# Optimization experiments

Hardware: AMD Instinct MI355X
Metric: run time of the kernel (lower is better)

The kernel has to match this reference:

```python
import jax, jax.numpy as jnp
import numpy as np

V, E, H, K = 50000, 256, 512, 32
START, STOP = 30, 31
B, T = 32, 256
NEG = -10000.0


def _lstm_dir(x, W_ih, W_hh, b, h0, c0):
    # x: [T,B,E] -> outputs [T,B,H]; PyTorch gate order i,f,g,o
    xw = jnp.einsum('tbe,ge->tbg', x, W_ih) + b  # [T,B,4H]
    def step(carry, xw_t):
        h, c = carry
        z = xw_t + h @ W_hh.T
        i, f, g, o = jnp.split(z, 4, axis=-1)
        c = jax.nn.sigmoid(f) * c + jax.nn.sigmoid(i) * jnp.tanh(g)
        h = jax.nn.sigmoid(o) * jnp.tanh(c)
        return (h, c), h
    (_, _), hs = jax.lax.scan(step, (h0, c0), xw)
    return hs


def setup_inputs() -> dict:
    key = jax.random.key(0)
    ks = jax.random.split(key, 13)
    sc = 0.05
    sentence = jax.random.randint(ks[0], (B, T), 0, V)
    emb = jax.random.normal(ks[1], (V, E), jnp.float32) * 0.1
    W_ih_f = jax.random.normal(ks[2], (4 * H, E), jnp.float32) * sc
    W_hh_f = jax.random.normal(ks[3], (4 * H, H), jnp.float32) * sc
    b_f = jax.random.normal(ks[4], (4 * H,), jnp.float32) * sc
    W_ih_b = jax.random.normal(ks[5], (4 * H, E), jnp.float32) * sc
    W_hh_b = jax.random.normal(ks[6], (4 * H, H), jnp.float32) * sc
    b_b = jax.random.normal(ks[7], (4 * H,), jnp.float32) * sc
    W_out = jax.random.normal(ks[8], (K, 2 * H), jnp.float32) * sc
    b_out = jax.random.normal(ks[9], (K,), jnp.float32) * sc
    transitions = jax.random.normal(ks[10], (K, K), jnp.float32)
    transitions = transitions.at[START, :].set(NEG).at[:, STOP].set(NEG)
    h0 = jax.random.normal(ks[11], (2, B, H), jnp.float32)
    c0 = jax.random.normal(ks[12], (2, B, H), jnp.float32)
    return dict(sentence=sentence, emb=emb, W_ih_f=W_ih_f, W_hh_f=W_hh_f, b_f=b_f,
                W_ih_b=W_ih_b, W_hh_b=W_hh_b, b_b=b_b, W_out=W_out, b_out=b_out,
                transitions=transitions, h0=h0, c0=c0)


def reference(sentence, emb, W_ih_f, W_hh_f, b_f, W_ih_b, W_hh_b, b_b,
              W_out, b_out, transitions, h0, c0):
    batch, seqlen = sentence.shape
    ntag = transitions.shape[0]
    # embedding (dropout = identity at inference), time-major
    x = emb[sentence].transpose(1, 0, 2)  # [T,B,E]
    hf = _lstm_dir(x, W_ih_f, W_hh_f, b_f, h0[0], c0[0])
    hb = _lstm_dir(x[::-1], W_ih_b, W_hh_b, b_b, h0[1], c0[1])[::-1]
    rnn_out = jnp.concatenate([hf, hb], axis=-1).transpose(1, 0, 2)  # [B,T,2H]
    feats = rnn_out @ W_out.T + b_out  # [B,T,K]

    # Viterbi decode, vectorized over batch and tags
    v0 = jnp.full((batch, ntag), NEG, feats.dtype).at[:, START].set(0.0)
    def vstep(v, feat_t):
        # scores[b, next, prev] = v[b, prev] + transitions[next, prev]
        scores = v[:, None, :] + transitions[None, :, :]
        bp = jnp.argmax(scores, axis=-1)              # [B,K] best prev per next
        v_new = jnp.max(scores, axis=-1) + feat_t     # [B,K]
        return v_new, bp
    v, bps = jax.lax.scan(vstep, v0, feats.transpose(1, 0, 2))  # bps: [T,B,K]

    terminal = v + transitions[STOP]                  # [B,K]
    best_last = jnp.argmax(terminal, axis=-1)         # [B]
    path_score = jnp.take_along_axis(terminal, best_last[:, None], axis=1)[:, 0]

    def back(tag, bp_t):
        prev = jnp.take_along_axis(bp_t, tag[:, None], axis=1)[:, 0]
        return prev, tag
    _, path = jax.lax.scan(back, best_last, bps, reverse=True)  # [T,B], time order
    best_path = path.transpose(1, 0)                  # [B,T]
    return path_score, best_path
```

## Files before the change

kernel.cpp:

```cpp
#include <hip/hip_runtime.h>
#include <hip/hip_bf16.h>
#include <cstdint>


typedef __attribute__((ext_vector_type(8)))  short          s8v;
typedef __attribute__((ext_vector_type(8)))  __bf16         bf8v;
typedef __attribute__((ext_vector_type(16))) float          f32x16;
typedef __attribute__((ext_vector_type(4)))  float          f32x4v;
typedef __attribute__((ext_vector_type(4)))  unsigned int   u32x4;
typedef __attribute__((ext_vector_type(8)))  unsigned short u16x8;
typedef __attribute__((ext_vector_type(4)))  unsigned short u16x4;

template <typename V>
static __device__ inline auto mfma_try(V a, V b, f32x16 c, int)
    -> decltype(__builtin_amdgcn_mfma_f32_32x32x16_bf16(a, b, c, 0, 0, 0)) {
  return __builtin_amdgcn_mfma_f32_32x32x16_bf16(a, b, c, 0, 0, 0);
}
template <typename V>
static __device__ inline f32x16 mfma_try(V a, V b, f32x16 c, long) {
  return __builtin_amdgcn_mfma_f32_32x32x16_bf16(
      __builtin_bit_cast(bf8v, a), __builtin_bit_cast(bf8v, b), c, 0, 0, 0);
}
static __device__ inline f32x16 mfma32(u16x8 a, u16x8 b, f32x16 c) {
  return mfma_try(__builtin_bit_cast(s8v, a), __builtin_bit_cast(s8v, b), c, 0);
}

static __device__ inline unsigned short bf_trunc(float x) {
  return (unsigned short)(__builtin_bit_cast(unsigned int, x) >> 16);
}
static __device__ inline float bf_up(unsigned short h) {
  return __builtin_bit_cast(float, ((unsigned int)h) << 16);
}
static __device__ inline void split2(float x, unsigned short& hi, unsigned short& lo) {
  hi = bf_trunc(x);
  lo = bf_trunc(x - bf_up(hi));
}
static __device__ inline float sigmoidf_(float x) { return 1.0f / (1.0f + __expf(-x)); }
static __device__ inline float tanhf_(float x) {
  float ax = fabsf(x);
  float e  = __expf(-2.0f * ax);
  float t  = (1.0f - e) / (1.0f + e);
  return x < 0.0f ? -t : t;
}

static __device__ inline u32x4 ld16(const void* p) {
  u32x4 r;
  asm volatile("global_load_dwordx4 %0, %1, off" : "=v"(r) : "v"(p) : "memory");
  return r;
}
static __device__ inline u32x4 ld_cohere16(const void* p) {
  u32x4 r;
  asm volatile("global_load_dwordx4 %0, %1, off sc0 sc1" : "=v"(r) : "v"(p) : "memory");
  return r;
}
static __device__ inline void st_cohere16(void* p, u32x4 v) {
  asm volatile("global_store_dwordx4 %0, %1, off sc0 sc1" :: "v"(p), "v"(v) : "memory");
}
static __device__ inline void st_cohere4(void* p, int v) {
  asm volatile("global_store_dword %0, %1, off sc0 sc1" :: "v"(p), "v"(v) : "memory");
}
#define WAITVM(N)                                              \
  do {                                                         \
    asm volatile("s_waitcnt vmcnt(" #N ")" ::: "memory");      \
    __builtin_amdgcn_sched_barrier(0);                         \
  } while (0)

__global__ void k_embed(const int* __restrict__ sent, const float* __restrict__ emb,
                        unsigned short* __restrict__ xhi, unsigned short* __restrict__ xlo) {
  int row  = blockIdx.x * 4 + (threadIdx.x >> 6);
  int lane = threadIdx.x & 63;
  int t = row >> 5, b = row & 31;
  int tok = sent[b * 256 + t];
  const f32x4v v = *(const f32x4v*)(emb + (long)tok * 256 + lane * 4);
  u16x4 h4, l4;
#pragma unroll
  for (int i = 0; i < 4; ++i) {
    unsigned short h, l;
    split2(v[i], h, l);
    h4[i] = h; l4[i] = l;
  }
  *(u16x4*)(xhi + (long)row * 256 + lane * 4) = h4;
  *(u16x4*)(xlo + (long)row * 256 + lane * 4) = l4;
}

__global__ __launch_bounds__(256, 1) void k_lstm(
    const float* __restrict__ Whh_f, const float* __restrict__ Whh_b,
    const float* __restrict__ Wih_f, const float* __restrict__ Wih_b,
    const float* __restrict__ b_f,   const float* __restrict__ b_b,
    const float* __restrict__ h0,    const float* __restrict__ c0,
    const unsigned short* __restrict__ xhi, const unsigned short* __restrict__ xlo,
    unsigned short* __restrict__ hist, int* __restrict__ flags) {
  const int tid = threadIdx.x, lane = tid & 63, w = tid >> 6;
  const int blk = blockIdx.x, dir = blk >> 6, b64 = blk & 63;
  const float* Whh  = dir ? Whh_b : Whh_f;
  const float* Wih  = dir ? Wih_b : Wih_f;
  const float* bias = dir ? b_b   : b_f;

  __shared__ float zp[4][32][33];
  __shared__ __align__(16) unsigned short hstage[512];

  const int n  = lane & 31;
  const int kh = lane >> 5;
  const int wrow = ((n >> 3) << 9) + (b64 << 3) + (n & 7);

  u16x8 wbh[8], wbl[8];
#pragma unroll
  for (int k8 = 0; k8 < 8; ++k8) {
    const float* src = Whh + (long)wrow * 512 + (w << 7) + (k8 << 4) + (kh << 3);
    f32x4v a = *(const f32x4v*)src, b2 = *(const f32x4v*)(src + 4);
    u16x8 hh, ll;
#pragma unroll
    for (int i = 0; i < 8; ++i) {
      float v = (i < 4) ? a[i] : b2[i - 4];
      unsigned short x1, x2; split2(v, x1, x2);
      hh[i] = x1; ll[i] = x2;
    }
    wbh[k8] = hh; wbl[k8] = ll;
  }
  u16x8 wih_h[4], wih_l[4];
#pragma unroll
  for (int k4 = 0; k4 < 4; ++k4) {
    const float* src = Wih + (long)wrow * 256 + (w << 6) + (k4 << 4) + (kh << 3);
    f32x4v a = *(const f32x4v*)src, b2 = *(const f32x4v*)(src + 4);
    u16x8 hh, ll;
#pragma unroll
    for (int i = 0; i < 8; ++i) {
      float v = (i < 4) ? a[i] : b2[i - 4];
      unsigned short x1, x2; split2(v, x1, x2);
      hh[i] = x1; ll[i] = x2;
    }
    wih_h[k4] = hh; wih_l[k4] = ll;
  }

  const int gb = tid & 31;
  const int gi = tid >> 5;
  const int gidx = (b64 << 3) + gi;
  float c = c0[(dir * 32 + gb) * 512 + gidx];
  float bias4[4];
#pragma unroll
  for (int g = 0; g < 4; ++g) bias4[g] = bias[(g << 9) + gidx];

  {
    float hv = h0[(dir * 32 + gb) * 512 + gidx];
    unsigned short hh, ll; split2(hv, hh, ll);
    hstage[gb * 8 + gi] = hh;
    hstage[256 + gb * 8 + gi] = ll;
  }
  __syncthreads();
  if (w == 0) {
    const u32x4* hs = (const u32x4*)hstage;
    u32x4 v = hs[lane];
    char* dst = (char*)hist + (((long)dir * 257 + 0) * 64 + b64) * 1024 + lane * 16;
    st_cohere16(dst, v);
    WAITVM(0);
  }
  __syncthreads();
  if (tid == 0) st_cohere4(flags + dir * 64 + b64, 1);

  const int m = lane & 31;

  u32x4 xah_[4], xal_[4];
  {
    const int t0 = dir ? 255 : 0;
#pragma unroll
    for (int k4 = 0; k4 < 4; ++k4) {
      long ro = (long)(t0 * 32 + m) * 256 + (w << 6) + (k4 << 4) + (kh << 3);
      xah_[k4] = ld16(xhi + ro);
      xal_[k4] = ld16(xlo + ro);
    }
  }

  for (int step = 0; step < 256; ++step) {
    WAITVM(0);
    f32x16 acc0 = (f32x16)0.0f, acc1 = (f32x16)0.0f;
#pragma unroll
    for (int k4 = 0; k4 < 4; ++k4) {
      u16x8 xa = __builtin_bit_cast(u16x8, xah_[k4]);
      u16x8 xl = __builtin_bit_cast(u16x8, xal_[k4]);
      if (k4 & 1) {
        acc1 = mfma32(xa, wih_h[k4], acc1);
        acc0 = mfma32(xa, wih_l[k4], acc0);
        acc1 = mfma32(xl, wih_h[k4], acc1);
      } else {
        acc0 = mfma32(xa, wih_h[k4], acc0);
        acc1 = mfma32(xa, wih_l[k4], acc1);
        acc0 = mfma32(xl, wih_h[k4], acc0);
      }
    }
    __builtin_amdgcn_sched_barrier(0);

    {
      const int* fl = flags + dir * 64;
      const int tgt = step + 1;
      while (true) {
        int fv = __hip_atomic_load(fl + lane, __ATOMIC_RELAXED, __HIP_MEMORY_SCOPE_AGENT);
        if (__all(fv >= tgt)) break;
      }
    }

    const unsigned short* hb = hist + (((long)dir * 257 + step) * 64) * 512;
    u32x4 ah_[8], al_[8];
#pragma unroll
    for (int k8 = 0; k8 < 8; ++k8) {
      int bs = (w << 4) + (k8 << 1) + kh;
      ah_[k8] = ld_cohere16(hb + bs * 512 + m * 8);
      al_[k8] = ld_cohere16(hb + bs * 512 + 256 + m * 8);
    }

    WAITVM(8);
#pragma unroll
    for (int k8 = 0; k8 < 4; ++k8) {
      u16x8 ah = __builtin_bit_cast(u16x8, ah_[k8]);
      u16x8 al = __builtin_bit_cast(u16x8, al_[k8]);
      if (k8 & 1) {
        acc1 = mfma32(ah, wbh[k8], acc1);
        acc0 = mfma32(ah, wbl[k8], acc0);
        acc1 = mfma32(al, wbh[k8], acc1);
      } else {
        acc0 = mfma32(ah, wbh[k8], acc0);
        acc1 = mfma32(ah, wbl[k8], acc1);
        acc0 = mfma32(al, wbh[k8], acc0);
      }
    }
    WAITVM(0);
#pragma unroll
    for (int k8 = 4; k8 < 8; ++k8) {
      u16x8 ah = __builtin_bit_cast(u16x8, ah_[k8]);
      u16x8 al = __builtin_bit_cast(u16x8, al_[k8]);
      if (k8 & 1) {
        acc1 = mfma32(ah, wbh[k8], acc1);
        acc0 = mfma32(ah, wbl[k8], acc0);
        acc1 = mfma32(al, wbh[k8], acc1);
      } else {
        acc0 = mfma32(ah, wbh[k8], acc0);
        acc1 = mfma32(ah, wbl[k8], acc1);
        acc0 = mfma32(al, wbh[k8], acc0);
      }
    }

#pragma unroll
    for (int r = 0; r < 16; ++r) {
      int mr = (r & 3) + ((r >> 2) << 3) + (kh << 2);
      zp[w][mr][n] = acc0[r] + acc1[r];
    }
    __syncthreads();

    float z[4];
#pragma unroll
    for (int g = 0; g < 4; ++g)
      z[g] = zp[0][gb][g * 8 + gi] + zp[1][gb][g * 8 + gi] +
             zp[2][gb][g * 8 + gi] + zp[3][gb][g * 8 + gi] + bias4[g];
    float ig = sigmoidf_(z[0]);
    float fg = sigmoidf_(z[1]);
    float gg = tanhf_(z[2]);
    float og = sigmoidf_(z[3]);
    c = fg * c + ig * gg;
    float nh = og * tanhf_(c);
    unsigned short hh, ll; split2(nh, hh, ll);

    if (step < 255) {
      const int tn = dir ? (254 - step) : (step + 1);
#pragma unroll
      for (int k4 = 0; k4 < 4; ++k4) {
        long ro = (long)(tn * 32 + m) * 256 + (w << 6) + (k4 << 4) + (kh << 3);
        xah_[k4] = ld16(xhi + ro);
        xal_[k4] = ld16(xlo + ro);
      }
    }

    hstage[gb * 8 + gi] = hh;
    hstage[256 + gb * 8 + gi] = ll;
    __syncthreads();
    if (w == 0) {
      const u32x4* hs = (const u32x4*)hstage;
      u32x4 v = hs[lane];
      char* dst = (char*)hist + (((long)dir * 257 + step + 1) * 64 + b64) * 1024 + lane * 16;
      st_cohere16(dst, v);
      WAITVM(0);
    }
    __syncthreads();
    if (tid == 0) st_cohere4(flags + dir * 64 + b64, step + 2);
  }
}

__global__ __launch_bounds__(256, 1) void k_feats(
    const unsigned short* __restrict__ hist,
    const float* __restrict__ Wout, const float* __restrict__ bout,
    float* __restrict__ feats) {
  const int tid = threadIdx.x, lane = tid & 63, w = tid >> 6;
  const int t = blockIdx.x;
  __shared__ float zp[4][32][33];
  const int n = lane & 31, kh = lane >> 5;
  const int dirw = w >> 1, koff = (w & 1) * 256;

  u16x8 bh[16], bl[16];
#pragma unroll
  for (int k = 0; k < 16; ++k) {
    const float* src = Wout + (long)n * 1024 + dirw * 512 + koff + (k << 4) + (kh << 3);
    f32x4v a = *(const f32x4v*)src, b2 = *(const f32x4v*)(src + 4);
    u16x8 hh, ll;
#pragma unroll
    for (int i = 0; i < 8; ++i) {
      float v = (i < 4) ? a[i] : b2[i - 4];
      unsigned short x1, x2; split2(v, x1, x2);
      hh[i] = x1; ll[i] = x2;
    }
    bh[k] = hh; bl[k] = ll;
  }

  const int m = lane & 31;
  const int slot = dirw ? (256 - t) : (t + 1);
  const unsigned short* base = hist + (((long)dirw * 257 + slot) * 64) * 512;
  f32x16 acc = (f32x16)0.0f;
#pragma unroll
  for (int k = 0; k < 16; ++k) {
    int ksrc = koff + (k << 4) + (kh << 3);
    int bs = ksrc >> 3;
    u16x8 ah = *(const u16x8*)(base + bs * 512 + m * 8);
    u16x8 al = *(const u16x8*)(base + bs * 512 + 256 + m * 8);
    acc = mfma32(ah, bh[k], acc);
    acc = mfma32(ah, bl[k], acc);
    acc = mfma32(al, bh[k], acc);
  }
#pragma unroll
  for (int r = 0; r < 16; ++r) {
    int mr = (r & 3) + ((r >> 2) << 3) + (kh << 2);
    zp[w][mr][n] = acc[r];
  }
  __syncthreads();

  const int k = tid & 31, mb = tid >> 5;
#pragma unroll
  for (int q = 0; q < 4; ++q) {
    int mm = mb * 4 + q;
    float v = zp[0][mm][k] + zp[1][mm][k] + zp[2][mm][k] + zp[3][mm][k] + bout[k];
    feats[((long)mm * 256 + t) * 32 + k] = v;
  }
}

__global__ __launch_bounds__(64, 1) void k_viterbi(const float* __restrict__ feats,
                                                   const float* __restrict__ trans,
                                                   float* __restrict__ out) {
  const int b = blockIdx.x, lane = threadIdx.x;
  __shared__ __align__(16) float fsh[256][32];
  __shared__ unsigned char bp[256][32];

  const float* fb = feats + (long)b * 8192;
#pragma unroll 4
  for (int i = lane; i < 2048; i += 64)
    ((f32x4v*)&fsh[0][0])[i] = ((const f32x4v*)fb)[i];

  float tr_[32];
  float vl = 0.0f;
  if (lane < 32) {
#pragma unroll
    for (int p = 0; p < 32; ++p) tr_[p] = trans[lane * 32 + p];
    vl = (lane == 30) ? 0.0f : -10000.0f;
  }
  __syncthreads();

  if (lane < 32) {
    for (int t = 0; t < 256; ++t) {
      float best = -3.0e38f; int arg = 0;
#pragma unroll
      for (int p = 0; p < 32; ++p) {
        float vp = __shfl(vl, p, 32);
        float sc = vp + tr_[p];
        if (sc > best) { best = sc; arg = p; }
      }
      vl = best + fsh[t][lane];
      bp[t][lane] = (unsigned char)arg;
    }
    float tv = vl + trans[31 * 32 + lane];
    int ta = lane;
#pragma unroll
    for (int d = 16; d; d >>= 1) {
      float ov = __shfl_xor(tv, d, 32);
      int   oa = __shfl_xor(ta, d, 32);
      if (ov > tv || (ov == tv && oa < ta)) { tv = ov; ta = oa; }
    }
    if (lane == 0) {
      out[b] = tv;
      int tag = ta;
      for (int t = 255; t >= 0; --t) {
        out[32 + (long)b * 256 + t] = (float)tag;
        tag = bp[t][tag];
      }
    }
  }
}

extern "C" void kernel_launch(void* const* d_in, const int* in_sizes, int n_in,
                              void* d_out, int out_size, void* d_ws, size_t ws_size,
                              hipStream_t stream) {
  (void)in_sizes; (void)n_in; (void)out_size; (void)ws_size;
  const int*   sent  = (const int*)d_in[0];
  const float* emb   = (const float*)d_in[1];
  const float* Wih_f = (const float*)d_in[2];
  const float* Whh_f = (const float*)d_in[3];
  const float* b_f   = (const float*)d_in[4];
  const float* Wih_b = (const float*)d_in[5];
  const float* Whh_b = (const float*)d_in[6];
  const float* b_b   = (const float*)d_in[7];
  const float* Wout  = (const float*)d_in[8];
  const float* bout  = (const float*)d_in[9];
  const float* trans = (const float*)d_in[10];
  const float* h0    = (const float*)d_in[11];
  const float* c0    = (const float*)d_in[12];
  float* out = (float*)d_out;

  char* ws = (char*)d_ws;
  unsigned short* xhi  = (unsigned short*)(ws + 0);
  unsigned short* xlo  = (unsigned short*)(ws + (4ull << 20));
  unsigned short* hist = (unsigned short*)(ws + (8ull << 20));
  float*          fts  = (float*)(ws + (42ull << 20));
  int*            flg  = (int*)(ws + (44ull << 20));

  hipMemsetAsync(flg, 0, 128 * sizeof(int), stream);
  k_embed<<<2048, 256, 0, stream>>>(sent, emb, xhi, xlo);
  k_lstm<<<128, 256, 0, stream>>>(Whh_f, Whh_b, Wih_f, Wih_b, b_f, b_b, h0, c0,
                                  xhi, xlo, hist, flg);
  k_feats<<<256, 256, 0, stream>>>(hist, Wout, bout, fts);
  k_viterbi<<<32, 64, 0, stream>>>(fts, trans, out);
}
```

Baseline: 1.542 ms.

## Pre-split LSTM weight fragments in a prep kernel and overlap input MFMAs with h loads

Adds a k_wprep kernel that converts the recurrent and input weights into bf16 hi/lo MFMA fragments once, so each LSTM block loads ready fragments instead of splitting fp32 weights itself. Inside the recurrent loop, the input-projection MFMAs now run after the cross-block flag wait, overlapping with the coherent loads of the previous hidden state. Each wave polls only 16 flags. The trailing __syncthreads before the flag store is removed, and the hstage layout and gate-thread mapping are changed. This costs an extra kernel launch and workspace traffic, and it changes the synchronisation order inside the step.

```diff
diff --git a/kernel.cpp b/kernel.cpp
--- a/kernel.cpp
+++ b/kernel.cpp
@@ -21,7 +21,7 @@
   return __builtin_amdgcn_mfma_f32_32x32x16_bf16(
       __builtin_bit_cast(bf8v, a), __builtin_bit_cast(bf8v, b), c, 0, 0, 0);
 }
-static __device__ inline f32x16 mfma32(u16x8 a, u16x8 b, f32x16 c) {
+static __device__ inline f32x16 mfma32(u32x4 a, u32x4 b, f32x16 c) {
   return mfma_try(__builtin_bit_cast(s8v, a), __builtin_bit_cast(s8v, b), c, 0);
 }
 
@@ -83,81 +83,74 @@
   *(u16x4*)(xlo + (long)row * 256 + lane * 4) = l4;
 }
 
+__global__ void k_wprep(const float* __restrict__ Whh_f, const float* __restrict__ Whh_b,
+                        const float* __restrict__ Wih_f, const float* __restrict__ Wih_b,
+                        unsigned short* __restrict__ wfrag) {
+  unsigned int g = blockIdx.x * 256 + threadIdx.x;
+  int lane = g & 63;
+  unsigned int r = g >> 6;
+  int f = r % 24; r /= 24;
+  int w = r & 3;  r >>= 2;
+  int b64 = r & 63;
+  int dir = (int)(r >> 6);
+  int n = lane & 31, kh = lane >> 5;
+  int wrow = ((n >> 3) << 9) + (b64 << 3) + (n & 7);
+  const float* src;
+  bool hi;
+  if (f < 16) {
+    int k8 = f & 7; hi = (f < 8);
+    src = (dir ? Whh_b : Whh_f) + (long)wrow * 512 + (w << 7) + (k8 << 4) + (kh << 3);
+  } else {
+    int k4 = (f - 16) & 3; hi = (f < 20);
+    src = (dir ? Wih_b : Wih_f) + (long)wrow * 256 + (w << 6) + (k4 << 4) + (kh << 3);
+  }
+  f32x4v a = *(const f32x4v*)src, b2 = *(const f32x4v*)(src + 4);
+  u16x8 o;
+#pragma unroll
+  for (int i = 0; i < 8; ++i) {
+    float v = (i < 4) ? a[i] : b2[i - 4];
+    unsigned short h, l; split2(v, h, l);
+    o[i] = hi ? h : l;
+  }
+  *(u16x8*)(wfrag + (long)g * 8) = o;
+}
+
 __global__ __launch_bounds__(256, 1) void k_lstm(
-    const float* __restrict__ Whh_f, const float* __restrict__ Whh_b,
-    const float* __restrict__ Wih_f, const float* __restrict__ Wih_b,
-    const float* __restrict__ b_f,   const float* __restrict__ b_b,
-    const float* __restrict__ h0,    const float* __restrict__ c0,
+    const float* __restrict__ b_f, const float* __restrict__ b_b,
+    const float* __restrict__ h0,  const float* __restrict__ c0,
     const unsigned short* __restrict__ xhi, const unsigned short* __restrict__ xlo,
+    const unsigned short* __restrict__ wfrag,
     unsigned short* __restrict__ hist, int* __restrict__ flags) {
   const int tid = threadIdx.x, lane = tid & 63, w = tid >> 6;
   const int blk = blockIdx.x, dir = blk >> 6, b64 = blk & 63;
-  const float* Whh  = dir ? Whh_b : Whh_f;
-  const float* Wih  = dir ? Wih_b : Wih_f;
-  const float* bias = dir ? b_b   : b_f;
+  const float* bias = dir ? b_b : b_f;
 
   __shared__ float zp[4][32][33];
   __shared__ __align__(16) unsigned short hstage[512];
 
-  const int n  = lane & 31;
   const int kh = lane >> 5;
-  const int wrow = ((n >> 3) << 9) + (b64 << 3) + (n & 7);
-
-  u16x8 wbh[8], wbl[8];
-#pragma unroll
-  for (int k8 = 0; k8 < 8; ++k8) {
-    const float* src = Whh + (long)wrow * 512 + (w << 7) + (k8 << 4) + (kh << 3);
-    f32x4v a = *(const f32x4v*)src, b2 = *(const f32x4v*)(src + 4);
-    u16x8 hh, ll;
-#pragma unroll
-    for (int i = 0; i < 8; ++i) {
-      float v = (i < 4) ? a[i] : b2[i - 4];
-      unsigned short x1, x2; split2(v, x1, x2);
-      hh[i] = x1; ll[i] = x2;
-    }
-    wbh[k8] = hh; wbl[k8] = ll;
-  }
-  u16x8 wih_h[4], wih_l[4];
-#pragma unroll
-  for (int k4 = 0; k4 < 4; ++k4) {
-    const float* src = Wih + (long)wrow * 256 + (w << 6) + (k4 << 4) + (kh << 3);
-    f32x4v a = *(const f32x4v*)src, b2 = *(const f32x4v*)(src + 4);
-    u16x8 hh, ll;
-#pragma unroll
-    for (int i = 0; i < 8; ++i) {
-      float v = (i < 4) ? a[i] : b2[i - 4];
-      unsigned short x1, x2; split2(v, x1, x2);
-      hh[i] = x1; ll[i] = x2;
-    }
-    wih_h[k4] = hh; wih_l[k4] = ll;
-  }
-
-  const int gb = tid & 31;
-  const int gi = tid >> 5;
+  const int m  = lane & 31;
+
+  const unsigned short* wf =
+      wfrag + (((long)(dir * 64 + b64) * 4 + w) * 24) * 64 * 8;
+  u32x4 wbh[8], wbl[8], wihh[4], wihl[4];
+#pragma unroll
+  for (int k8 = 0; k8 < 8; ++k8) wbh[k8] = ld16(wf + ((k8)*64 + lane) * 8);
+#pragma unroll
+  for (int k8 = 0; k8 < 8; ++k8) wbl[k8] = ld16(wf + ((8 + k8) * 64 + lane) * 8);
+#pragma unroll
+  for (int k4 = 0; k4 < 4; ++k4) wihh[k4] = ld16(wf + ((16 + k4) * 64 + lane) * 8);
+#pragma unroll
+  for (int k4 = 0; k4 < 4; ++k4) wihl[k4] = ld16(wf + ((20 + k4) * 64 + lane) * 8);
+  WAITVM(0);
+
+  const int gb = tid >> 3;
+  const int gi = tid & 7;
   const int gidx = (b64 << 3) + gi;
   float c = c0[(dir * 32 + gb) * 512 + gidx];
   float bias4[4];
 #pragma unroll
   for (int g = 0; g < 4; ++g) bias4[g] = bias[(g << 9) + gidx];
-
-  {
-    float hv = h0[(dir * 32 + gb) * 512 + gidx];
-    unsigned short hh, ll; split2(hv, hh, ll);
-    hstage[gb * 8 + gi] = hh;
-    hstage[256 + gb * 8 + gi] = ll;
-  }
-  __syncthreads();
-  if (w == 0) {
-    const u32x4* hs = (const u32x4*)hstage;
-    u32x4 v = hs[lane];
-    char* dst = (char*)hist + (((long)dir * 257 + 0) * 64 + b64) * 1024 + lane * 16;
-    st_cohere16(dst, v);
-    WAITVM(0);
-  }
-  __syncthreads();
-  if (tid == 0) st_cohere4(flags + dir * 64 + b64, 1);
-
-  const int m = lane & 31;
 
   u32x4 xah_[4], xal_[4];
   {
@@ -170,30 +163,28 @@
     }
   }
 
+  {
+    float hv = h0[(dir * 32 + gb) * 512 + gidx];
+    unsigned short hh, ll; split2(hv, hh, ll);
+    hstage[tid] = hh;
+    hstage[256 + tid] = ll;
+  }
+  __syncthreads();
+  if (w == 0) {
+    u32x4 v = ((const u32x4*)hstage)[lane];
+    char* dst = (char*)hist + (((long)dir * 257 + 0) * 64 + b64) * 1024 + lane * 16;
+    st_cohere16(dst, v);
+    WAITVM(0);
+    if (lane == 0) st_cohere4(flags + dir * 64 + b64, 1);
+  }
+
   for (int step = 0; step < 256; ++step) {
-    WAITVM(0);
-    f32x16 acc0 = (f32x16)0.0f, acc1 = (f32x16)0.0f;
-#pragma unroll
-    for (int k4 = 0; k4 < 4; ++k4) {
-      u16x8 xa = __builtin_bit_cast(u16x8, xah_[k4]);
-      u16x8 xl = __builtin_bit_cast(u16x8, xal_[k4]);
-      if (k4 & 1) {
-        acc1 = mfma32(xa, wih_h[k4], acc1);
-        acc0 = mfma32(xa, wih_l[k4], acc0);
-        acc1 = mfma32(xl, wih_h[k4], acc1);
-      } else {
-        acc0 = mfma32(xa, wih_h[k4], acc0);
-        acc1 = mfma32(xa, wih_l[k4], acc1);
-        acc0 = mfma32(xl, wih_h[k4], acc0);
-      }
-    }
-    __builtin_amdgcn_sched_barrier(0);
-
     {
-      const int* fl = flags + dir * 64;
+      const int* fl = flags + dir * 64 + (w << 4);
       const int tgt = step + 1;
       while (true) {
-        int fv = __hip_atomic_load(fl + lane, __ATOMIC_RELAXED, __HIP_MEMORY_SCOPE_AGENT);
+        int fv = __hip_atomic_load(fl + (lane & 15), __ATOMIC_RELAXED,
+                                   __HIP_MEMORY_SCOPE_AGENT);
         if (__all(fv >= tgt)) break;
       }
     }
@@ -207,37 +198,49 @@
       al_[k8] = ld_cohere16(hb + bs * 512 + 256 + m * 8);
     }
 
+    WAITVM(16);
+    f32x16 acc0 = (f32x16)0.0f, acc1 = (f32x16)0.0f;
+#pragma unroll
+    for (int k4 = 0; k4 < 4; ++k4) {
+      if (k4 & 1) {
+        acc1 = mfma32(xah_[k4], wihh[k4], acc1);
+        acc0 = mfma32(xah_[k4], wihl[k4], acc0);
+        acc1 = mfma32(xal_[k4], wihh[k4], acc1);
+      } else {
+        acc0 = mfma32(xah_[k4], wihh[k4], acc0);
+        acc1 = mfma32(xah_[k4], wihl[k4], acc1);
+        acc0 = mfma32(xal_[k4], wihh[k4], acc0);
+      }
+    }
+
     WAITVM(8);
 #pragma unroll
     for (int k8 = 0; k8 < 4; ++k8) {
-      u16x8 ah = __builtin_bit_cast(u16x8, ah_[k8]);
-      u16x8 al = __builtin_bit_cast(u16x8, al_[k8]);
       if (k8 & 1) {
-        acc1 = mfma32(ah, wbh[k8], acc1);
-        acc0 = mfma32(ah, wbl[k8], acc0);
-        acc1 = mfma32(al, wbh[k8], acc1);
+        acc1 = mfma32(ah_[k8], wbh[k8], acc1);
+        acc0 = mfma32(ah_[k8], wbl[k8], acc0);
+        acc1 = mfma32(al_[k8], wbh[k8], acc1);
       } else {
-        acc0 = mfma32(ah, wbh[k8], acc0);
-        acc1 = mfma32(ah, wbl[k8], acc1);
-        acc0 = mfma32(al, wbh[k8], acc0);
+        acc0 = mfma32(ah_[k8], wbh[k8], acc0);
+        acc1 = mfma32(ah_[k8], wbl[k8], acc1);
+        acc0 = mfma32(al_[k8], wbh[k8], acc0);
       }
     }
     WAITVM(0);
 #pragma unroll
     for (int k8 = 4; k8 < 8; ++k8) {
-      u16x8 ah = __builtin_bit_cast(u16x8, ah_[k8]);
-      u16x8 al = __builtin_bit_cast(u16x8, al_[k8]);
       if (k8 & 1) {
-        acc1 = mfma32(ah, wbh[k8], acc1);
-        acc0 = mfma32(ah, wbl[k8], acc0);
-        acc1 = mfma32(al, wbh[k8], acc1);
+        acc1 = mfma32(ah_[k8], wbh[k8], acc1);
+        acc0 = mfma32(ah_[k8], wbl[k8], acc0);
+        acc1 = mfma32(al_[k8], wbh[k8], acc1);
       } else {
-        acc0 = mfma32(ah, wbh[k8], acc0);
-        acc1 = mfma32(ah, wbl[k8], acc1);
-        acc0 = mfma32(al, wbh[k8], acc0);
-      }
-    }
-
+        acc0 = mfma32(ah_[k8], wbh[k8], acc0);
+        acc1 = mfma32(ah_[k8], wbl[k8], acc1);
+        acc0 = mfma32(al_[k8], wbh[k8], acc0);
+      }
+    }
+
+    const int n = lane & 31;
 #pragma unroll
     for (int r = 0; r < 16; ++r) {
       int mr = (r & 3) + ((r >> 2) << 3) + (kh << 2);
@@ -268,18 +271,17 @@
       }
     }
 
-    hstage[gb * 8 + gi] = hh;
-    hstage[256 + gb * 8 + gi] = ll;
+    hstage[tid] = hh;
+    hstage[256 + tid] = ll;
     __syncthreads();
     if (w == 0) {
-      const u32x4* hs = (const u32x4*)hstage;
-      u32x4 v = hs[lane];
-      char* dst = (char*)hist + (((long)dir * 257 + step + 1) * 64 + b64) * 1024 + lane * 16;
+      u32x4 v = ((const u32x4*)hstage)[lane];
+      char* dst =
+          (char*)hist + (((long)dir * 257 + step + 1) * 64 + b64) * 1024 + lane * 16;
       st_cohere16(dst, v);
       WAITVM(0);
-    }
-    __syncthreads();
-    if (tid == 0) st_cohere4(flags + dir * 64 + b64, step + 2);
+      if (lane == 0) st_cohere4(flags + dir * 64 + b64, step + 2);
+    }
   }
 }
 
@@ -316,11 +318,11 @@
   for (int k = 0; k < 16; ++k) {
     int ksrc = koff + (k << 4) + (kh << 3);
     int bs = ksrc >> 3;
-    u16x8 ah = *(const u16x8*)(base + bs * 512 + m * 8);
-    u16x8 al = *(const u16x8*)(base + bs * 512 + 256 + m * 8);
-    acc = mfma32(ah, bh[k], acc);
-    acc = mfma32(ah, bl[k], acc);
-    acc = mfma32(al, bh[k], acc);
+    u32x4 ah = *(const u32x4*)(base + bs * 512 + m * 8);
+    u32x4 al = *(const u32x4*)(base + bs * 512 + 256 + m * 8);
+    acc = mfma32(ah, __builtin_bit_cast(u32x4, bh[k]), acc);
+    acc = mfma32(ah, __builtin_bit_cast(u32x4, bl[k]), acc);
+    acc = mfma32(al, __builtin_bit_cast(u32x4, bh[k]), acc);
   }
 #pragma unroll
   for (int r = 0; r < 16; ++r) {
@@ -410,16 +412,17 @@
   float* out = (float*)d_out;
 
   char* ws = (char*)d_ws;
-  unsigned short* xhi  = (unsigned short*)(ws + 0);
-  unsigned short* xlo  = (unsigned short*)(ws + (4ull << 20));
-  unsigned short* hist = (unsigned short*)(ws + (8ull << 20));
-  float*          fts  = (float*)(ws + (42ull << 20));
-  int*            flg  = (int*)(ws + (44ull << 20));
+  unsigned short* xhi   = (unsigned short*)(ws + 0);
+  unsigned short* xlo   = (unsigned short*)(ws + (4ull << 20));
+  unsigned short* hist  = (unsigned short*)(ws + (8ull << 20));
+  unsigned short* wfrag = (unsigned short*)(ws + (41ull << 20));
+  float*          fts   = (float*)(ws + (54ull << 20));
+  int*            flg   = (int*)(ws + (55ull << 20) + (512ull << 10));
 
   hipMemsetAsync(flg, 0, 128 * sizeof(int), stream);
   k_embed<<<2048, 256, 0, stream>>>(sent, emb, xhi, xlo);
-  k_lstm<<<128, 256, 0, stream>>>(Whh_f, Whh_b, Wih_f, Wih_b, b_f, b_b, h0, c0,
-                                  xhi, xlo, hist, flg);
+  k_wprep<<<3072, 256, 0, stream>>>(Whh_f, Whh_b, Wih_f, Wih_b, wfrag);
+  k_lstm<<<128, 256, 0, stream>>>(b_f, b_b, h0, c0, xhi, xlo, wfrag, hist, flg);
   k_feats<<<256, 256, 0, stream>>>(hist, Wout, bout, fts);
   k_viterbi<<<32, 64, 0, stream>>>(fts, trans, out);
 }
```

Result: slower. 2.161 ms (+40.1%).
